# Optimization experiments

Hardware: AMD Instinct MI355X
Metric: run time of the kernel (lower is better)

## Reference

```python
import jax, jax.numpy as jnp
import numpy as np

B, C, H, W = 16, 15, 256, 256

def setup_inputs() -> dict:
    key = jax.random.key(0)
    k1, k2, k3 = jax.random.split(key, 3)
    output = jax.random.normal(k1, (B, C, H, W), dtype=jnp.float32)
    label0 = jax.random.normal(k2, (B, C, H, W), dtype=jnp.float32)
    label1 = jax.random.uniform(k3, (B, C, H, W), dtype=jnp.float32)
    return {"output": output, "label0": label0, "label1": label1}

def reference(output, label0, label1):
    # Fused masked-L1 reduction over the whole tensor (replaces per-(b,c) loop)
    loss = jnp.sum(jnp.abs(output - label0) * label1)
    nonzero_num = jnp.sum(label0 != 0)  # total count of nonzero target entries
    # if nonzero_num == 0: loss -> 0, denom -> 1
    safe_denom = jnp.where(nonzero_num == 0, 1, nonzero_num).astype(loss.dtype)
    loss = jnp.where(nonzero_num == 0, jnp.zeros_like(loss), loss)
    return loss / safe_denom
```

## Files before the change

kernel.cpp:

```cpp
#include <hip/hip_runtime.h>
#include <hip/hip_bf16.h>


#define REDUCE_THREADS 256
#define REDUCE_BLOCKS 2048

struct Partial {
    float s;
    unsigned int c;
};

__device__ __forceinline__ void accum(const float4& o, const float4& a,
                                      const float4& w, float& sum,
                                      unsigned int& cnt) {
    sum += fabsf(o.x - a.x) * w.x;
    sum += fabsf(o.y - a.y) * w.y;
    sum += fabsf(o.z - a.z) * w.z;
    sum += fabsf(o.w - a.w) * w.w;
    cnt += (a.x != 0.0f) + (a.y != 0.0f) + (a.z != 0.0f) + (a.w != 0.0f);
}

__global__ __launch_bounds__(REDUCE_THREADS, 8)
void depth_loss_stage1(const float4* __restrict__ out,
                       const float4* __restrict__ l0,
                       const float4* __restrict__ l1,
                       Partial* __restrict__ partials,
                       int n4) {
    const int stride = gridDim.x * REDUCE_THREADS;
    int i = blockIdx.x * REDUCE_THREADS + threadIdx.x;

    float sum = 0.0f;
    unsigned int cnt = 0;

    if (i < n4) {
        float4 o0 = out[i];
        float4 a0 = l0[i];
        float4 w0 = l1[i];
        int j = i + stride;
        #pragma unroll 2
        for (; j < n4; j += stride) {
            float4 o1 = out[j];
            float4 a1 = l0[j];
            float4 w1 = l1[j];
            accum(o0, a0, w0, sum, cnt);
            o0 = o1; a0 = a1; w0 = w1;
        }
        accum(o0, a0, w0, sum, cnt);
    }

    #pragma unroll
    for (int off = 32; off > 0; off >>= 1) {
        sum += __shfl_down(sum, off, 64);
        cnt += __shfl_down(cnt, off, 64);
    }

    __shared__ float        sv[REDUCE_THREADS / 64];
    __shared__ unsigned int sc[REDUCE_THREADS / 64];
    int lane = threadIdx.x & 63;
    int wid  = threadIdx.x >> 6;
    if (lane == 0) { sv[wid] = sum; sc[wid] = cnt; }
    __syncthreads();

    if (threadIdx.x == 0) {
        float bs = 0.0f;
        unsigned int bc = 0;
        #pragma unroll
        for (int k = 0; k < REDUCE_THREADS / 64; ++k) { bs += sv[k]; bc += sc[k]; }
        Partial p; p.s = bs; p.c = bc;
        partials[blockIdx.x] = p;
    }
}

__global__ __launch_bounds__(REDUCE_THREADS)
void depth_loss_stage2(const Partial* __restrict__ partials,
                       int nblocks,
                       float* __restrict__ out) {
    double sum = 0.0;
    unsigned int cnt = 0;
    for (int i = threadIdx.x; i < nblocks; i += REDUCE_THREADS) {
        Partial p = partials[i];
        sum += (double)p.s;
        cnt += p.c;
    }

    #pragma unroll
    for (int off = 32; off > 0; off >>= 1) {
        sum += __shfl_down(sum, off, 64);
        cnt += __shfl_down(cnt, off, 64);
    }

    __shared__ double       sv[REDUCE_THREADS / 64];
    __shared__ unsigned int sc[REDUCE_THREADS / 64];
    int lane = threadIdx.x & 63;
    int wid  = threadIdx.x >> 6;
    if (lane == 0) { sv[wid] = sum; sc[wid] = cnt; }
    __syncthreads();

    if (threadIdx.x == 0) {
        double bs = 0.0;
        unsigned int bc = 0;
        #pragma unroll
        for (int k = 0; k < REDUCE_THREADS / 64; ++k) { bs += sv[k]; bc += sc[k]; }
        out[0] = (bc == 0) ? 0.0f : (float)(bs / (double)bc);
    }
}

extern "C" void kernel_launch(void* const* d_in, const int* in_sizes, int n_in,
                              void* d_out, int out_size, void* d_ws, size_t ws_size,
                              hipStream_t stream) {
    const float* output = (const float*)d_in[0];
    const float* label0 = (const float*)d_in[1];
    const float* label1 = (const float*)d_in[2];
    int n = in_sizes[0];
    int n4 = n >> 2;

    Partial* partials = (Partial*)d_ws;

    depth_loss_stage1<<<REDUCE_BLOCKS, REDUCE_THREADS, 0, stream>>>(
        (const float4*)output, (const float4*)label0, (const float4*)label1,
        partials, n4);

    depth_loss_stage2<<<1, REDUCE_THREADS, 0, stream>>>(
        partials, REDUCE_BLOCKS, (float*)d_out);
}
```

Before: 189.0 us.

## Software-pipeline stage1 loads with fixed-iteration unrolled ring buffer

Replaces the grid-stride loop with a fully unrolled fixed eight-iteration loop that keeps three iterations of float4 loads in flight via a four-slot register ring, with a sched_barrier to preserve ordering. Only the last iteration is bounds-checked. This aims to raise memory-level parallelism for the bandwidth-bound reduction, at the cost of more registers (occupancy hint lowered to 6) and hardcoding the trip count to the problem size.

New measurement: 189.3 us. No clear change (+0.1%).

```diff
diff --git a/kernel.cpp b/kernel.cpp
--- a/kernel.cpp
+++ b/kernel.cpp
@@ -2,8 +2,12 @@
 #include <hip/hip_bf16.h>
 
 
-#define REDUCE_THREADS 256
-#define REDUCE_BLOCKS 2048
+#define THREADS 256
+#define BLOCKS  2048
+#define SSTRIDE (BLOCKS * THREADS)
+#define ITERS   8
+#define NBUF    4
+#define DIST    3
 
 struct Partial {
     float s;
@@ -20,32 +24,46 @@
     cnt += (a.x != 0.0f) + (a.y != 0.0f) + (a.z != 0.0f) + (a.w != 0.0f);
 }
 
-__global__ __launch_bounds__(REDUCE_THREADS, 8)
+__global__ __launch_bounds__(THREADS, 6)
 void depth_loss_stage1(const float4* __restrict__ out,
                        const float4* __restrict__ l0,
                        const float4* __restrict__ l1,
                        Partial* __restrict__ partials,
                        int n4) {
-    const int stride = gridDim.x * REDUCE_THREADS;
-    int i = blockIdx.x * REDUCE_THREADS + threadIdx.x;
+    const int tid = blockIdx.x * THREADS + threadIdx.x;
+    const int tail_n = n4 - (ITERS - 1) * SSTRIDE;
+
+    float4 o[NBUF], a[NBUF], w[NBUF];
+
+    #pragma unroll
+    for (int k = 0; k < DIST; ++k) {
+        int j = tid + k * SSTRIDE;
+        o[k] = out[j];
+        a[k] = l0[j];
+        w[k] = l1[j];
+    }
 
     float sum = 0.0f;
     unsigned int cnt = 0;
 
-    if (i < n4) {
-        float4 o0 = out[i];
-        float4 a0 = l0[i];
-        float4 w0 = l1[i];
-        int j = i + stride;
-        #pragma unroll 2
-        for (; j < n4; j += stride) {
-            float4 o1 = out[j];
-            float4 a1 = l0[j];
-            float4 w1 = l1[j];
-            accum(o0, a0, w0, sum, cnt);
-            o0 = o1; a0 = a1; w0 = w1;
+    #pragma unroll
+    for (int k = 0; k < ITERS; ++k) {
+        const int kp = k + DIST;
+        if (kp < ITERS) {
+            int j = tid + kp * SSTRIDE;
+            if (kp == ITERS - 1) j = (tid < tail_n) ? j : tid;
+            const int s = kp & (NBUF - 1);
+            o[s] = out[j];
+            a[s] = l0[j];
+            w[s] = l1[j];
         }
-        accum(o0, a0, w0, sum, cnt);
+        __builtin_amdgcn_sched_barrier(0);
+        const int s = k & (NBUF - 1);
+        if (k == ITERS - 1) {
+            if (tid < tail_n) accum(o[s], a[s], w[s], sum, cnt);
+        } else {
+            accum(o[s], a[s], w[s], sum, cnt);
+        }
     }
 
     #pragma unroll
@@ -54,8 +72,8 @@
         cnt += __shfl_down(cnt, off, 64);
     }
 
-    __shared__ float        sv[REDUCE_THREADS / 64];
-    __shared__ unsigned int sc[REDUCE_THREADS / 64];
+    __shared__ float        sv[THREADS / 64];
+    __shared__ unsigned int sc[THREADS / 64];
     int lane = threadIdx.x & 63;
     int wid  = threadIdx.x >> 6;
     if (lane == 0) { sv[wid] = sum; sc[wid] = cnt; }
@@ -65,19 +83,19 @@
         float bs = 0.0f;
         unsigned int bc = 0;
         #pragma unroll
-        for (int k = 0; k < REDUCE_THREADS / 64; ++k) { bs += sv[k]; bc += sc[k]; }
+        for (int k = 0; k < THREADS / 64; ++k) { bs += sv[k]; bc += sc[k]; }
         Partial p; p.s = bs; p.c = bc;
         partials[blockIdx.x] = p;
     }
 }
 
-__global__ __launch_bounds__(REDUCE_THREADS)
+__global__ __launch_bounds__(THREADS)
 void depth_loss_stage2(const Partial* __restrict__ partials,
                        int nblocks,
                        float* __restrict__ out) {
     double sum = 0.0;
     unsigned int cnt = 0;
-    for (int i = threadIdx.x; i < nblocks; i += REDUCE_THREADS) {
+    for (int i = threadIdx.x; i < nblocks; i += THREADS) {
         Partial p = partials[i];
         sum += (double)p.s;
         cnt += p.c;
@@ -89,8 +107,8 @@
         cnt += __shfl_down(cnt, off, 64);
     }
 
-    __shared__ double       sv[REDUCE_THREADS / 64];
-    __shared__ unsigned int sc[REDUCE_THREADS / 64];
+    __shared__ double       sv[THREADS / 64];
+    __shared__ unsigned int sc[THREADS / 64];
     int lane = threadIdx.x & 63;
     int wid  = threadIdx.x >> 6;
     if (lane == 0) { sv[wid] = sum; sc[wid] = cnt; }
@@ -100,7 +118,7 @@
         double bs = 0.0;
         unsigned int bc = 0;
         #pragma unroll
-        for (int k = 0; k < REDUCE_THREADS / 64; ++k) { bs += sv[k]; bc += sc[k]; }
+        for (int k = 0; k < THREADS / 64; ++k) { bs += sv[k]; bc += sc[k]; }
         out[0] = (bc == 0) ? 0.0f : (float)(bs / (double)bc);
     }
 }
@@ -116,10 +134,10 @@
 
     Partial* partials = (Partial*)d_ws;
 
-    depth_loss_stage1<<<REDUCE_BLOCKS, REDUCE_THREADS, 0, stream>>>(
+    depth_loss_stage1<<<BLOCKS, THREADS, 0, stream>>>(
         (const float4*)output, (const float4*)label0, (const float4*)label1,
         partials, n4);
 
-    depth_loss_stage2<<<1, REDUCE_THREADS, 0, stream>>>(
-        partials, REDUCE_BLOCKS, (float*)d_out);
+    depth_loss_stage2<<<1, THREADS, 0, stream>>>(
+        partials, BLOCKS, (float*)d_out);
 }
```
